# Performance work log

Measured on AMD Instinct MI355X. Metric: run time of the kernel, lower is better.

Reference implementation:

```python
import jax, jax.numpy as jnp
import numpy as np
import math

H = 768
NH = 12
DK = H // NH
EPS = 1e-12

def gelu(x):
    return 0.5 * x * (1 + jnp.tanh(math.sqrt(2 / math.pi) * (x + 0.044715 * x ** 3)))

def layernorm(x, w, b):
    u = x.mean(-1, keepdims=True)
    s = ((x - u) ** 2).mean(-1, keepdims=True)
    return w * (x - u) / jnp.sqrt(s + EPS) + b

def setup_inputs() -> dict:
    key = jax.random.key(0)
    ks = jax.random.split(key, 12)
    B, S = 4, 2048
    std = 1.0 / math.sqrt(H)
    inp = {
        'x': jax.random.normal(ks[0], (B, S, H), jnp.float32),
        'mask': jax.random.randint(ks[1], (B, S), 0, 2, jnp.int32),
        'wq': jax.random.normal(ks[2], (H, H), jnp.float32) * std,
        'wk': jax.random.normal(ks[3], (H, H), jnp.float32) * std,
        'wv': jax.random.normal(ks[4], (H, H), jnp.float32) * std,
        'wo': jax.random.normal(ks[5], (H, H), jnp.float32) * std,
        'wo_b': jnp.zeros((H,), jnp.float32),
        'w1': jax.random.normal(ks[6], (H, 4 * H), jnp.float32) * std,
        'w1_b': jnp.zeros((4 * H,), jnp.float32),
        'w2': jax.random.normal(ks[7], (4 * H, H), jnp.float32) * (0.5 / math.sqrt(H)),
        'w2_b': jnp.zeros((H,), jnp.float32),
        'ln1_w': jnp.ones((H,), jnp.float32),
        'ln1_b': jnp.zeros((H,), jnp.float32),
        'ln2_w': jnp.ones((H,), jnp.float32),
        'ln2_b': jnp.zeros((H,), jnp.float32),
    }
    return inp

def reference(x, mask, wq, wk, wv, wo, wo_b, w1, w1_b, w2, w2_b, ln1_w, ln1_b, ln2_w, ln2_b):
    B, S, _ = x.shape
    # --- attention sublayer (pre-LN, residual) ---
    y = layernorm(x, ln1_w, ln1_b)
    q = (y @ wq).reshape(B, S, NH, DK).transpose(0, 2, 1, 3)
    k = (y @ wk).reshape(B, S, NH, DK).transpose(0, 2, 1, 3)
    v = (y @ wv).reshape(B, S, NH, DK).transpose(0, 2, 1, 3)
    scores = jnp.einsum('bhqd,bhkd->bhqk', q, k) / math.sqrt(DK)
    m2 = (mask[:, :, None] * mask[:, None, :])[:, None, :, :]  # [B,1,S,S]
    scores = jnp.where(m2 == 0, jnp.float32(-1e9), scores)
    p = jax.nn.softmax(scores, axis=-1)
    ctx = jnp.einsum('bhqk,bhkd->bhqd', p, v).transpose(0, 2, 1, 3).reshape(B, S, H)
    x = x + ctx @ wo + wo_b
    # --- FFN sublayer ---
    y2 = layernorm(x, ln2_w, ln2_b)
    x = x + gelu(y2 @ w1 + w1_b) @ w2 + w2_b
    return x
```

## Files before the change

kernel.cpp:

```cpp
#include <hip/hip_runtime.h>
#include <hip/hip_bf16.h>

#define HD   768
#define BSZ  4
#define SEQ  2048
#define NTOK (BSZ*SEQ)
#define NHD  12
#define DKD  64

typedef __bf16 bf16_t;
typedef __bf16 bf16x8 __attribute__((ext_vector_type(8)));
typedef __bf16 bf16x4 __attribute__((ext_vector_type(4)));
typedef float  f32x4  __attribute__((ext_vector_type(4)));

__device__ __forceinline__ void async16(const void* g, void* l) {
    __builtin_amdgcn_global_load_lds(
        (const __attribute__((address_space(1))) unsigned int*)g,
        (__attribute__((address_space(3))) unsigned int*)l, 16, 0, 0);
}

__global__ __launch_bounds__(256) void prep_kernel(
    const float* __restrict__ wq, const float* __restrict__ wk,
    const float* __restrict__ wv, const float* __restrict__ wo,
    const float* __restrict__ w1, const float* __restrict__ w2,
    const int* __restrict__ mask,
    bf16_t* __restrict__ wqkvT, bf16_t* __restrict__ woT,
    bf16_t* __restrict__ w1T, bf16_t* __restrict__ w2T,
    float* __restrict__ mb)
{
    const int bid = blockIdx.x, t = threadIdx.x;
    if (bid >= 6912) {
        const int i = (bid - 6912) * 256 + t;
        mb[i] = mask[i] ? 0.f : -1e9f;
        return;
    }
    const float* in; bf16_t* out; int K, N, ktile, ntile;
    if (bid < 2304) {
        const int wsel = bid / 576, tt = bid % 576;
        const float* srcs[4] = { wq, wk, wv, wo };
        bf16_t* dsts[4] = { wqkvT, wqkvT + 768*768, wqkvT + 2*768*768, woT };
        in = srcs[wsel]; out = dsts[wsel]; K = 768; N = 768;
        ktile = tt / 24; ntile = tt % 24;
    } else if (bid < 4608) {
        const int tt = bid - 2304;
        in = w1; out = w1T; K = 768; N = 3072;
        ktile = tt / 96; ntile = tt % 96;
    } else {
        const int tt = bid - 4608;
        in = w2; out = w2T; K = 3072; N = 768;
        ktile = tt / 24; ntile = tt % 24;
    }
    __shared__ float tile[32][33];
    const int k0 = ktile * 32, n0 = ntile * 32;
    const int r = t >> 5, c = t & 31;
#pragma unroll
    for (int j = 0; j < 4; j++)
        tile[r + 8*j][c] = in[(size_t)(k0 + r + 8*j) * N + n0 + c];
    __syncthreads();
#pragma unroll
    for (int j = 0; j < 4; j++)
        out[(size_t)(n0 + r + 8*j) * K + k0 + c] = (bf16_t)tile[c][r + 8*j];
}

__global__ __launch_bounds__(256) void ln_kernel(
    const float* __restrict__ x, const float* __restrict__ gw,
    const float* __restrict__ gb, bf16_t* __restrict__ y)
{
    const int row = blockIdx.x, t = threadIdx.x;
    const float* xr = x + (size_t)row * HD;
    float v0 = xr[t], v1 = xr[t + 256], v2 = xr[t + 512];
    float s1 = v0 + v1 + v2;
    float s2 = v0*v0 + v1*v1 + v2*v2;
#pragma unroll
    for (int m = 1; m < 64; m <<= 1) {
        s1 += __shfl_xor(s1, m);
        s2 += __shfl_xor(s2, m);
    }
    __shared__ float red[8];
    const int w = t >> 6, l = t & 63;
    if (l == 0) { red[w] = s1; red[4 + w] = s2; }
    __syncthreads();
    s1 = red[0] + red[1] + red[2] + red[3];
    s2 = red[4] + red[5] + red[6] + red[7];
    float mean = s1 * (1.f/HD);
    float var  = fmaxf(s2 * (1.f/HD) - mean*mean, 0.f);
    float rstd = rsqrtf(var + 1e-12f);
    bf16_t* yr = y + (size_t)row * HD;
    yr[t]       = (bf16_t)(gw[t]      * (v0 - mean) * rstd + gb[t]);
    yr[t + 256] = (bf16_t)(gw[t + 256]* (v1 - mean) * rstd + gb[t + 256]);
    yr[t + 512] = (bf16_t)(gw[t + 512]* (v2 - mean) * rstd + gb[t + 512]);
}

template<int EPI>
__global__ __launch_bounds__(256) void gemm_bt(
    const bf16_t* __restrict__ A, const bf16_t* __restrict__ BT,
    const float* __restrict__ bias, const float* __restrict__ resid,
    void* __restrict__ outv, int M, int N, int K, int ldo,
    bf16_t* __restrict__ vtout)
{
    __shared__ __align__(16) unsigned char lds[49152];
    const int t = threadIdx.x;
    const int w = t >> 6, l = t & 63;
    const int wr = w >> 1, wc = w & 1;
    const int lr = l & 15, lg = l >> 4;
    const int nwg = gridDim.x * gridDim.y;
    int flat = blockIdx.y * gridDim.x + blockIdx.x;
    flat = (flat & 7) * (nwg >> 3) + (flat >> 3);
    const int bx = flat % gridDim.x, by = flat / gridDim.x;
    const int m0 = by * 128, n0 = bx * 128;

    const bf16_t* a_src = A  + (size_t)(m0 + (t >> 2)) * K + (t & 3) * 8;
    const bf16_t* b_src = BT + (size_t)(n0 + (t >> 2)) * K + (t & 3) * 8;
    f32x4 acc[4][4] = {};

    auto stage = [&](int kt, int buf) {
        unsigned char* d = lds + buf * 16384 + t * 16;
        async16(a_src + kt,                 d);
        async16(a_src + (size_t)64*K + kt,  d + 4096);
        async16(b_src + kt,                 d + 8192);
        async16(b_src + (size_t)64*K + kt,  d + 12288);
    };

    const int nt = K >> 5;
    stage(0, 0);
    stage(32, 1);
    asm volatile("s_waitcnt vmcnt(4)" ::: "memory");
    __builtin_amdgcn_s_barrier();

    int cur = 0;
    for (int it = 0; it < nt; ++it) {
        const bool pre = (it + 2 < nt);
        if (pre) {
            int b2 = cur + 2; if (b2 >= 3) b2 -= 3;
            stage((it + 2) << 5, b2);
        }
        const unsigned char* bufp = lds + cur * 16384;
        bf16x8 af[4], bfr[4];
#pragma unroll
        for (int n = 0; n < 4; n++)
            bfr[n] = *(const bf16x8*)(bufp + 8192 + (wc*64 + n*16 + lr)*64 + lg*16);
#pragma unroll
        for (int m = 0; m < 4; m++)
            af[m] = *(const bf16x8*)(bufp + (wr*64 + m*16 + lr)*64 + lg*16);
        __builtin_amdgcn_s_setprio(1);
#pragma unroll
        for (int m = 0; m < 4; m++)
#pragma unroll
            for (int n = 0; n < 4; n++)
                acc[m][n] = __builtin_amdgcn_mfma_f32_16x16x32_bf16(af[m], bfr[n], acc[m][n], 0, 0, 0);
        __builtin_amdgcn_s_setprio(0);
        if (it + 1 < nt) {
            asm volatile("s_waitcnt lgkmcnt(0)" ::: "memory");
            if (pre) asm volatile("s_waitcnt vmcnt(4)" ::: "memory");
            else     asm volatile("s_waitcnt vmcnt(0)" ::: "memory");
            __builtin_amdgcn_s_barrier();
        }
        cur = (cur + 1 == 3) ? 0 : cur + 1;
    }

#pragma unroll
    for (int m = 0; m < 4; m++) {
#pragma unroll
        for (int n = 0; n < 4; n++) {
            const int gc  = n0 + wc*64 + n*16 + lr;
            const int gr0 = m0 + wr*64 + m*16 + lg*4;
            if constexpr (EPI == 3) {
                if (gc >= 1536) {
                    const int hh = (gc - 1536) >> 6, dd = (gc - 1536) & 63;
                    const int bb = gr0 >> 11, ss = gr0 & 2047;
                    bf16x4 ov;
#pragma unroll
                    for (int i = 0; i < 4; i++) ov[i] = (bf16_t)acc[m][n][i];
                    *(bf16x4*)(vtout + ((size_t)(bb*NHD + hh)*64 + dd)*SEQ + ss) = ov;
                    continue;
                }
            }
#pragma unroll
            for (int i = 0; i < 4; i++) {
                const int gr = gr0 + i;
                float v = acc[m][n][i];
                if constexpr (EPI == 0 || EPI == 3) {
                    ((bf16_t*)outv)[(size_t)gr * ldo + gc] = (bf16_t)v;
                } else if constexpr (EPI == 1) {
                    ((float*)outv)[(size_t)gr * ldo + gc] =
                        v + bias[gc] + resid[(size_t)gr * ldo + gc];
                } else {
                    v += bias[gc];
                    float u = 0.7978845608028654f * (v + 0.044715f * v * v * v);
                    float g = v / (1.f + __expf(-2.f * u));
                    ((bf16_t*)outv)[(size_t)gr * ldo + gc] = (bf16_t)g;
                }
            }
        }
    }
}

__global__ __launch_bounds__(256) void attn_kernel(
    const bf16_t* __restrict__ qkv, const bf16_t* __restrict__ vt,
    const int* __restrict__ mask, const float* __restrict__ mbias,
    bf16_t* __restrict__ ctx)
{
    __shared__ __align__(16) unsigned char lds[49152];
    const int t = threadIdx.x, w = t >> 6, l = t & 63;
    const int lr = l & 15, lg = l >> 4;
    int flat = blockIdx.y * 16 + blockIdx.x;
    flat = (flat & 7) * 96 + (flat >> 3);
    const int bh = flat >> 4, qt = flat & 15;
    const int b = bh / NHD, h = bh % NHD;
    const int q0 = qt * 128 + w * 32;
    const int swz = (lr & 7) << 4;

    bf16x8 qf[2][2];
#pragma unroll
    for (int r = 0; r < 2; r++)
#pragma unroll
        for (int ks = 0; ks < 2; ks++)
            qf[r][ks] = *(const bf16x8*)(qkv + (size_t)(b*SEQ + q0 + r*16 + lr)*2304
                                         + h*64 + ks*32 + lg*8);
    int mq[2];
#pragma unroll
    for (int r = 0; r < 2; r++)
        mq[r] = mask[b*SEQ + q0 + r*16 + lr];

    float mrow[2] = { -INFINITY, -INFINITY };
    float lsum[2] = { 0.f, 0.f };
    f32x4 accO[2][4] = {};

    auto stage_kv = [&](int kt, int buf) {
        unsigned char* d = lds + buf * 16384;
#pragma unroll
        for (int i2 = 0; i2 < 2; i2++) {
            const int c = i2*256 + t;
            const int row = c >> 3;
            const int scol = ((c & 7) ^ (row & 7)) * 8;
            async16(qkv + (size_t)(b*SEQ + kt + row)*2304 + 768 + h*64 + scol,
                    d + c*16);
            async16(vt + ((size_t)bh*64 + row)*SEQ + kt + scol,
                    d + 8192 + c*16);
        }
    };

    stage_kv(0, 0);
    __syncthreads();

    int cur = 0;
    for (int kt = 0; kt < SEQ; kt += 64) {
        if (kt + 64 < SEQ) stage_kv(kt + 64, cur ^ 1);
        f32x4 mb[4];
#pragma unroll
        for (int n = 0; n < 4; n++)
            mb[n] = *(const f32x4*)(mbias + (size_t)b*SEQ + kt + n*16 + lg*4);
        const unsigned char* bufp = lds + cur * 16384;

        bf16x8 kf[4][2];
#pragma unroll
        for (int n = 0; n < 4; n++)
#pragma unroll
            for (int ks = 0; ks < 2; ks++)
                kf[n][ks] = *(const bf16x8*)(bufp + (n*16 + lr)*128
                                             + ((ks*64 + lg*16) ^ swz));
        f32x4 accS[4][2] = {};
        __builtin_amdgcn_s_setprio(1);
#pragma unroll
        for (int n = 0; n < 4; n++)
#pragma unroll
            for (int r = 0; r < 2; r++)
#pragma unroll
                for (int ks = 0; ks < 2; ks++)
                    accS[n][r] = __builtin_amdgcn_mfma_f32_16x16x32_bf16(
                        kf[n][ks], qf[r][ks], accS[n][r], 0, 0, 0);
        __builtin_amdgcn_s_setprio(0);

#pragma unroll
        for (int r = 0; r < 2; r++) {
            f32x4 sl[4];
#pragma unroll
            for (int n = 0; n < 4; n++)
#pragma unroll
                for (int i = 0; i < 4; i++)
                    sl[n][i] = mq[r] ? (accS[n][r][i] * 0.125f + mb[n][i]) : -1e9f;
            float px = -INFINITY;
#pragma unroll
            for (int n = 0; n < 4; n++)
                px = fmaxf(px, fmaxf(fmaxf(sl[n][0], sl[n][1]),
                                     fmaxf(sl[n][2], sl[n][3])));
            px = fmaxf(px, __shfl_xor(px, 16));
            px = fmaxf(px, __shfl_xor(px, 32));
            const float mold = mrow[r];
            if (!__all(px <= mold + 8.f)) {
                const float mnew = fmaxf(mold, px);
                const float sc = __expf(mold - mnew);
                lsum[r] *= sc;
#pragma unroll
                for (int dn = 0; dn < 4; dn++) accO[r][dn] *= sc;
                mrow[r] = mnew;
            }
            const float m = mrow[r];
            float ps = 0.f;
#pragma unroll
            for (int n = 0; n < 4; n++) {
                bf16x4 pk;
#pragma unroll
                for (int i = 0; i < 4; i++) {
                    float pv = __expf(sl[n][i] - m);
                    ps += pv;
                    pk[i] = (bf16_t)pv;
                }
                *(bf16x4*)(lds + 32768 + w*4096 + (r*16 + lr)*128
                           + ((n*32 + lg*8) ^ swz)) = pk;
            }
            ps += __shfl_xor(ps, 16);
            ps += __shfl_xor(ps, 32);
            lsum[r] += ps;
        }

        bf16x8 vf[4][2], pf[2][2];
#pragma unroll
        for (int dn = 0; dn < 4; dn++)
#pragma unroll
            for (int ks = 0; ks < 2; ks++)
                vf[dn][ks] = *(const bf16x8*)(bufp + 8192 + (dn*16 + lr)*128
                                              + ((ks*64 + lg*16) ^ swz));
#pragma unroll
        for (int r = 0; r < 2; r++)
#pragma unroll
            for (int ks = 0; ks < 2; ks++)
                pf[r][ks] = *(const bf16x8*)(lds + 32768 + w*4096 + (r*16 + lr)*128
                                             + ((ks*64 + lg*16) ^ swz));
        __builtin_amdgcn_s_setprio(1);
#pragma unroll
        for (int r = 0; r < 2; r++)
#pragma unroll
            for (int dn = 0; dn < 4; dn++)
#pragma unroll
                for (int ks = 0; ks < 2; ks++)
                    accO[r][dn] = __builtin_amdgcn_mfma_f32_16x16x32_bf16(
                        vf[dn][ks], pf[r][ks], accO[r][dn], 0, 0, 0);
        __builtin_amdgcn_s_setprio(0);

        __syncthreads();
        cur ^= 1;
    }

#pragma unroll
    for (int r = 0; r < 2; r++) {
        const float inv = 1.f / lsum[r];
#pragma unroll
        for (int dn = 0; dn < 4; dn++) {
            bf16x4 ov;
#pragma unroll
            for (int i = 0; i < 4; i++)
                ov[i] = (bf16_t)(accO[r][dn][i] * inv);
            *(bf16x4*)(ctx + (size_t)(b*SEQ + q0 + r*16 + lr)*HD
                       + h*64 + dn*16 + lg*4) = ov;
        }
    }
}

extern "C" void kernel_launch(void* const* d_in, const int* in_sizes, int n_in,
                              void* d_out, int out_size, void* d_ws, size_t ws_size,
                              hipStream_t stream)
{
    const float* x     = (const float*)d_in[0];
    const int*   mask  = (const int*)  d_in[1];
    const float* wq    = (const float*)d_in[2];
    const float* wk    = (const float*)d_in[3];
    const float* wv    = (const float*)d_in[4];
    const float* wo    = (const float*)d_in[5];
    const float* wo_b  = (const float*)d_in[6];
    const float* w1    = (const float*)d_in[7];
    const float* w1_b  = (const float*)d_in[8];
    const float* w2    = (const float*)d_in[9];
    const float* w2_b  = (const float*)d_in[10];
    const float* ln1_w = (const float*)d_in[11];
    const float* ln1_b = (const float*)d_in[12];
    const float* ln2_w = (const float*)d_in[13];
    const float* ln2_b = (const float*)d_in[14];

    unsigned char* ws = (unsigned char*)d_ws;
    size_t o = 0;
    auto alloc = [&](size_t bytes) {
        size_t r = o; o += (bytes + 255) & ~(size_t)255; return r;
    };
    bf16_t* wqkvT = (bf16_t*)(ws + alloc((size_t)2304*768*2));
    bf16_t* woT   = (bf16_t*)(ws + alloc((size_t)768*768*2));
    bf16_t* w1T   = (bf16_t*)(ws + alloc((size_t)3072*768*2));
    bf16_t* w2T   = (bf16_t*)(ws + alloc((size_t)768*3072*2));
    bf16_t* y     = (bf16_t*)(ws + alloc((size_t)NTOK*HD*2));
    float*  x1    = (float*) (ws + alloc((size_t)NTOK*HD*4));
    bf16_t* ctx   = (bf16_t*)(ws + alloc((size_t)NTOK*HD*2));
    float*  mbias = (float*) (ws + alloc((size_t)NTOK*4));
    bf16_t* qkv   = (bf16_t*)(ws + alloc((size_t)NTOK*2304*2));
    bf16_t* vt    = (bf16_t*)(ws + alloc((size_t)48*64*SEQ*2));
    bf16_t* hbuf  = qkv;
    (void)in_sizes; (void)n_in; (void)out_size; (void)ws_size;

    prep_kernel<<<6944,256,0,stream>>>(wq, wk, wv, wo, w1, w2, mask,
                                       wqkvT, woT, w1T, w2T, mbias);
    ln_kernel<<<NTOK,256,0,stream>>>(x, ln1_w, ln1_b, y);
    gemm_bt<3><<<dim3(18,64),256,0,stream>>>(y, wqkvT, nullptr, nullptr, qkv,
                                             NTOK, 2304, 768, 2304, vt);
    attn_kernel<<<dim3(16,48),256,0,stream>>>(qkv, vt, mask, mbias, ctx);
    gemm_bt<1><<<dim3(6,64),256,0,stream>>>(ctx, woT, wo_b, x, x1,
                                            NTOK, 768, 768, 768, nullptr);
    ln_kernel<<<NTOK,256,0,stream>>>(x1, ln2_w, ln2_b, y);
    gemm_bt<2><<<dim3(24,64),256,0,stream>>>(y, w1T, w1_b, nullptr, hbuf,
                                             NTOK, 3072, 768, 3072, nullptr);
    gemm_bt<1><<<dim3(6,64),256,0,stream>>>(hbuf, w2T, w2_b, x1, d_out,
                                            NTOK, 768, 3072, 768, nullptr);
}
```

Baseline: 413.7 us.

## Fold softmax scale into Wq, use exp2, defer row-sum reduction, merge LN1 into prep

Pre-multiplies Wq by log2(e)/sqrt(dk) during the weight transpose and scales the mask bias by log2(e), so the attention loop drops a multiply and can use exp2f. The row-sum shuffles inside the key loop are moved to the epilogue, done once per row. The first layernorm is folded into the prep kernel to save one launch. The rescale threshold is adjusted to the log2 domain, and the change adds a small rounding difference from scaling Wq before the bf16 conversion.

```diff
diff --git a/kernel.cpp b/kernel.cpp
--- a/kernel.cpp
+++ b/kernel.cpp
@@ -20,6 +20,8 @@
 }
 
 __global__ __launch_bounds__(256) void prep_kernel(
+    const float* __restrict__ x, const float* __restrict__ ln1_w,
+    const float* __restrict__ ln1_b, bf16_t* __restrict__ y,
     const float* __restrict__ wq, const float* __restrict__ wk,
     const float* __restrict__ wv, const float* __restrict__ wo,
     const float* __restrict__ w1, const float* __restrict__ w2,
@@ -29,24 +31,53 @@
     float* __restrict__ mb)
 {
     const int bid = blockIdx.x, t = threadIdx.x;
-    if (bid >= 6912) {
-        const int i = (bid - 6912) * 256 + t;
-        mb[i] = mask[i] ? 0.f : -1e9f;
+    if (bid < 8192) {
+        const int row = bid;
+        const float* xr = x + (size_t)row * HD;
+        float v0 = xr[t], v1 = xr[t + 256], v2 = xr[t + 512];
+        float s1 = v0 + v1 + v2;
+        float s2 = v0*v0 + v1*v1 + v2*v2;
+#pragma unroll
+        for (int m = 1; m < 64; m <<= 1) {
+            s1 += __shfl_xor(s1, m);
+            s2 += __shfl_xor(s2, m);
+        }
+        __shared__ float red[8];
+        const int w = t >> 6, l = t & 63;
+        if (l == 0) { red[w] = s1; red[4 + w] = s2; }
+        __syncthreads();
+        s1 = red[0] + red[1] + red[2] + red[3];
+        s2 = red[4] + red[5] + red[6] + red[7];
+        float mean = s1 * (1.f/HD);
+        float var  = fmaxf(s2 * (1.f/HD) - mean*mean, 0.f);
+        float rstd = rsqrtf(var + 1e-12f);
+        bf16_t* yr = y + (size_t)row * HD;
+        yr[t]       = (bf16_t)(ln1_w[t]      * (v0 - mean) * rstd + ln1_b[t]);
+        yr[t + 256] = (bf16_t)(ln1_w[t + 256]* (v1 - mean) * rstd + ln1_b[t + 256]);
+        yr[t + 512] = (bf16_t)(ln1_w[t + 512]* (v2 - mean) * rstd + ln1_b[t + 512]);
         return;
     }
+    const int wb = bid - 8192;
+    if (wb >= 6912) {
+        const int i = (wb - 6912) * 256 + t;
+        mb[i] = mask[i] ? 0.f : -1.4426950e9f;
+        return;
+    }
     const float* in; bf16_t* out; int K, N, ktile, ntile;
-    if (bid < 2304) {
-        const int wsel = bid / 576, tt = bid % 576;
+    float scale = 1.f;
+    if (wb < 2304) {
+        const int wsel = wb / 576, tt = wb % 576;
         const float* srcs[4] = { wq, wk, wv, wo };
         bf16_t* dsts[4] = { wqkvT, wqkvT + 768*768, wqkvT + 2*768*768, woT };
         in = srcs[wsel]; out = dsts[wsel]; K = 768; N = 768;
+        if (wsel == 0) scale = 0.18033688f;
         ktile = tt / 24; ntile = tt % 24;
-    } else if (bid < 4608) {
-        const int tt = bid - 2304;
+    } else if (wb < 4608) {
+        const int tt = wb - 2304;
         in = w1; out = w1T; K = 768; N = 3072;
         ktile = tt / 96; ntile = tt % 96;
     } else {
-        const int tt = bid - 4608;
+        const int tt = wb - 4608;
         in = w2; out = w2T; K = 3072; N = 768;
         ktile = tt / 24; ntile = tt % 24;
     }
@@ -59,7 +90,7 @@
     __syncthreads();
 #pragma unroll
     for (int j = 0; j < 4; j++)
-        out[(size_t)(n0 + r + 8*j) * K + k0 + c] = (bf16_t)tile[c][r + 8*j];
+        out[(size_t)(n0 + r + 8*j) * K + k0 + c] = (bf16_t)(tile[c][r + 8*j] * scale);
 }
 
 __global__ __launch_bounds__(256) void ln_kernel(
@@ -278,7 +309,7 @@
             for (int n = 0; n < 4; n++)
 #pragma unroll
                 for (int i = 0; i < 4; i++)
-                    sl[n][i] = mq[r] ? (accS[n][r][i] * 0.125f + mb[n][i]) : -1e9f;
+                    sl[n][i] = mq[r] ? (accS[n][r][i] + mb[n][i]) : -1e9f;
             float px = -INFINITY;
 #pragma unroll
             for (int n = 0; n < 4; n++)
@@ -287,9 +318,9 @@
             px = fmaxf(px, __shfl_xor(px, 16));
             px = fmaxf(px, __shfl_xor(px, 32));
             const float mold = mrow[r];
-            if (!__all(px <= mold + 8.f)) {
+            if (!__all(px <= mold + 11.54f)) {
                 const float mnew = fmaxf(mold, px);
-                const float sc = __expf(mold - mnew);
+                const float sc = exp2f(mold - mnew);
                 lsum[r] *= sc;
 #pragma unroll
                 for (int dn = 0; dn < 4; dn++) accO[r][dn] *= sc;
@@ -302,15 +333,13 @@
                 bf16x4 pk;
 #pragma unroll
                 for (int i = 0; i < 4; i++) {
-                    float pv = __expf(sl[n][i] - m);
+                    float pv = exp2f(sl[n][i] - m);
                     ps += pv;
                     pk[i] = (bf16_t)pv;
                 }
                 *(bf16x4*)(lds + 32768 + w*4096 + (r*16 + lr)*128
                            + ((n*32 + lg*8) ^ swz)) = pk;
             }
-            ps += __shfl_xor(ps, 16);
-            ps += __shfl_xor(ps, 32);
             lsum[r] += ps;
         }
 
@@ -344,7 +373,10 @@
 
 #pragma unroll
     for (int r = 0; r < 2; r++) {
-        const float inv = 1.f / lsum[r];
+        float ls = lsum[r];
+        ls += __shfl_xor(ls, 16);
+        ls += __shfl_xor(ls, 32);
+        const float inv = 1.f / ls;
 #pragma unroll
         for (int dn = 0; dn < 4; dn++) {
             bf16x4 ov;
@@ -395,9 +427,9 @@
     bf16_t* hbuf  = qkv;
     (void)in_sizes; (void)n_in; (void)out_size; (void)ws_size;
 
-    prep_kernel<<<6944,256,0,stream>>>(wq, wk, wv, wo, w1, w2, mask,
-                                       wqkvT, woT, w1T, w2T, mbias);
-    ln_kernel<<<NTOK,256,0,stream>>>(x, ln1_w, ln1_b, y);
+    prep_kernel<<<15136,256,0,stream>>>(x, ln1_w, ln1_b, y,
+                                        wq, wk, wv, wo, w1, w2, mask,
+                                        wqkvT, woT, w1T, w2T, mbias);
     gemm_bt<3><<<dim3(18,64),256,0,stream>>>(y, wqkvT, nullptr, nullptr, qkv,
                                              NTOK, 2304, 768, 2304, vt);
     attn_kernel<<<dim3(16,48),256,0,stream>>>(qkv, vt, mask, mbias, ctx);
```

After: 430.5 us. +4.1%, slower.
